# Kernel tuning notes

Hardware: AMD Instinct MI355X
Metric: run time of the kernel (lower is better)

The kernel has to match this reference:

```python
import jax, jax.numpy as jnp
import numpy as np

EPS = 1e-12  # torch F.normalize eps

def _normalize(x):
    # L2-normalize along last dim, matching F.normalize(dim=-1)
    n = jnp.linalg.norm(x, axis=-1, keepdims=True)
    return x / jnp.maximum(n, EPS)

def setup_inputs() -> dict:
    key = jax.random.key(0)
    k1, k2, k3 = jax.random.split(key, 3)
    B, K, D = 32768, 8, 256
    return {
        "drone_slots": jax.random.normal(k1, (B, K, D), dtype=jnp.float32),
        "sat_slots": jax.random.normal(k2, (B, K, D), dtype=jnp.float32),
        "labels": jax.random.randint(k3, (B,), 0, 1000, dtype=jnp.int64),
        "temperature": 0.1,
    }

def reference(drone_slots, sat_slots, labels, temperature):
    # labels are unused by the original math (targets are arange(K))
    ds = _normalize(drone_slots)  # [B,K,D]
    ss = _normalize(sat_slots)    # [B,K,D]
    logits = jnp.einsum("bkd,bjd->bkj", ds, ss) / temperature  # [B,K,K]
    # cross_entropy with targets = arange(K): positive is the diagonal
    lse = jax.nn.logsumexp(logits, axis=-1)                      # [B,K]
    pos = jnp.diagonal(logits, axis1=-2, axis2=-1)               # [B,K]
    ce_per_sample = jnp.mean(lse - pos, axis=-1)                 # [B], per-sample mean-reduced CE
    return jnp.mean(ce_per_sample)                               # average over batch
```

## Files before the change

### kernel.cpp

```cpp
#include <hip/hip_runtime.h>


typedef __attribute__((ext_vector_type(8))) short bf16x8;
typedef __attribute__((ext_vector_type(4))) float f32x4;

__device__ inline short f2bf(float f) {
  union { float f; unsigned u; } v; v.f = f;
  unsigned u = v.u;
  u += 0x7fffu + ((u >> 16) & 1u);
  return (short)(u >> 16);
}

extern "C" __global__ __launch_bounds__(256)
void slot_ce_mfma(const float* __restrict__ ds, const float* __restrict__ ss,
                  const float* __restrict__ tptr, float* __restrict__ ws,
                  int ntiles) {
  const int lane = threadIdx.x & 63;
  const int wid  = (blockIdx.x * (blockDim.x >> 6)) + (threadIdx.x >> 6);
  const int m = lane & 15;
  const int h = lane >> 4;
  const float inv_t = 1.0f / tptr[0];

  float loss = 0.0f;

  if (wid < ntiles) {
    const float4* pa = (const float4*)(ds + (size_t)wid * 4096);
    const float4* pb = (const float4*)(ss + (size_t)wid * 4096);
    const int base = m * 64 + h * 2;

    f32x4 acc = {0.f, 0.f, 0.f, 0.f};
    float ssqA = 0.f, ssqS = 0.f;

#pragma unroll
    for (int kb = 0; kb < 8; ++kb) {
      const int idx = base + kb * 8;
      float4 a0 = pa[idx], a1 = pa[idx + 1];
      float4 s0 = pb[idx], s1 = pb[idx + 1];

      ssqA += a0.x*a0.x + a0.y*a0.y + a0.z*a0.z + a0.w*a0.w
            + a1.x*a1.x + a1.y*a1.y + a1.z*a1.z + a1.w*a1.w;
      ssqS += s0.x*s0.x + s0.y*s0.y + s0.z*s0.z + s0.w*s0.w
            + s1.x*s1.x + s1.y*s1.y + s1.z*s1.z + s1.w*s1.w;

      bf16x8 af = { f2bf(a0.x), f2bf(a0.y), f2bf(a0.z), f2bf(a0.w),
                    f2bf(a1.x), f2bf(a1.y), f2bf(a1.z), f2bf(a1.w) };
      bf16x8 sf = { f2bf(s0.x), f2bf(s0.y), f2bf(s0.z), f2bf(s0.w),
                    f2bf(s1.x), f2bf(s1.y), f2bf(s1.z), f2bf(s1.w) };
      acc = __builtin_amdgcn_mfma_f32_16x16x32_bf16(af, sf, acc, 0, 0, 0);
    }

    ssqA += __shfl_xor(ssqA, 16, 64);
    ssqA += __shfl_xor(ssqA, 32, 64);
    ssqS += __shfl_xor(ssqS, 16, 64);
    ssqS += __shfl_xor(ssqS, 32, 64);
    float na0 = __shfl(ssqA, h * 4 + 0, 64);
    float na1 = __shfl(ssqA, h * 4 + 1, 64);
    float na2 = __shfl(ssqA, h * 4 + 2, 64);
    float na3 = __shfl(ssqA, h * 4 + 3, 64);

    float lg0 = acc[0] * rsqrtf(na0 * ssqS) * inv_t;
    float lg1 = acc[1] * rsqrtf(na1 * ssqS) * inv_t;
    float lg2 = acc[2] * rsqrtf(na2 * ssqS) * inv_t;
    float lg3 = acc[3] * rsqrtf(na3 * ssqS) * inv_t;

    float c = 0.0f;
#pragma unroll
    for (int r = 0; r < 4; ++r) {
      float lg = r == 0 ? lg0 : r == 1 ? lg1 : r == 2 ? lg2 : lg3;
      float mx = lg;
      mx = fmaxf(mx, __shfl_xor(mx, 1, 64));
      mx = fmaxf(mx, __shfl_xor(mx, 2, 64));
      mx = fmaxf(mx, __shfl_xor(mx, 4, 64));
      float e = __expf(lg - mx);
      e += __shfl_xor(e, 1, 64);
      e += __shfl_xor(e, 2, 64);
      e += __shfl_xor(e, 4, 64);
      float lse = mx + __logf(e);
      c += lse * 0.125f;
      if (4 * h + r == m) c -= lg;
    }
    if ((m >= 8) == (h >= 2)) loss = c;
  }

#pragma unroll
  for (int o = 32; o >= 1; o >>= 1) loss += __shfl_xor(loss, o, 64);
  __shared__ float red[4];
  if (lane == 0) red[threadIdx.x >> 6] = loss;
  __syncthreads();
  if (threadIdx.x == 0)
    ws[blockIdx.x] = (red[0] + red[1]) + (red[2] + red[3]);
}

extern "C" __global__ __launch_bounds__(256)
void slot_ce_finish(const float* __restrict__ ws, float* __restrict__ out,
                    int nparts, float scale) {
  __shared__ float red[256];
  float s = 0.0f;
  for (int i = threadIdx.x; i < nparts; i += 256) s += ws[i];
  red[threadIdx.x] = s;
  __syncthreads();
  for (int o = 128; o >= 1; o >>= 1) {
    if ((int)threadIdx.x < o) red[threadIdx.x] += red[threadIdx.x + o];
    __syncthreads();
  }
  if (threadIdx.x == 0) out[0] = red[0] * scale;
}

extern "C" void kernel_launch(void* const* d_in, const int* in_sizes, int n_in,
                              void* d_out, int out_size, void* d_ws, size_t ws_size,
                              hipStream_t stream) {
  const float* ds   = (const float*)d_in[0];
  const float* ss   = (const float*)d_in[1];
  const float* tptr = (const float*)d_in[3];
  float* out = (float*)d_out;
  float* ws  = (float*)d_ws;

  const int B      = in_sizes[0] / (8 * 256);
  const int ntiles = B / 2;
  const int blocks = (ntiles + 3) / 4;

  slot_ce_mfma<<<blocks, 256, 0, stream>>>(ds, ss, tptr, ws, ntiles);
  const float scale = 1.0f / (8.0f * (float)B);
  slot_ce_finish<<<1, 256, 0, stream>>>(ws, out, blocks, scale);
}
```

Before: 106.6 us.

## Hoist all tile loads up front and use packed bf16 conversion intrinsics

All 32 float4 loads per lane are issued before any compute, so every global load is in flight at once rather than interleaved with the MFMA loop. The manual round-to-nearest bf16 conversion is replaced by the __float22bfloat162_rn pair intrinsic, which may lower to packed conversion instructions on gfx950. The launch bounds gain a min-blocks hint of 2. Holding all 32 float4 values raises register pressure to about 128 VGPRs for loaded data, which could limit occupancy on this memory-bound kernel.

```diff
diff --git a/kernel.cpp b/kernel.cpp
--- a/kernel.cpp
+++ b/kernel.cpp
@@ -1,22 +1,27 @@
 #include <hip/hip_runtime.h>
+#include <hip/hip_bf16.h>
 
 
 typedef __attribute__((ext_vector_type(8))) short bf16x8;
 typedef __attribute__((ext_vector_type(4))) float f32x4;
 
-__device__ inline short f2bf(float f) {
-  union { float f; unsigned u; } v; v.f = f;
-  unsigned u = v.u;
-  u += 0x7fffu + ((u >> 16) & 1u);
-  return (short)(u >> 16);
+union BFPack { bf16x8 v; __hip_bfloat162 h[4]; };
+
+__device__ inline bf16x8 pack8(const float4& lo, const float4& hi) {
+  BFPack u;
+  u.h[0] = __float22bfloat162_rn(make_float2(lo.x, lo.y));
+  u.h[1] = __float22bfloat162_rn(make_float2(lo.z, lo.w));
+  u.h[2] = __float22bfloat162_rn(make_float2(hi.x, hi.y));
+  u.h[3] = __float22bfloat162_rn(make_float2(hi.z, hi.w));
+  return u.v;
 }
 
-extern "C" __global__ __launch_bounds__(256)
+extern "C" __global__ __launch_bounds__(256, 2)
 void slot_ce_mfma(const float* __restrict__ ds, const float* __restrict__ ss,
                   const float* __restrict__ tptr, float* __restrict__ ws,
                   int ntiles) {
   const int lane = threadIdx.x & 63;
-  const int wid  = (blockIdx.x * (blockDim.x >> 6)) + (threadIdx.x >> 6);
+  const int wid  = blockIdx.x * 4 + (threadIdx.x >> 6);
   const int m = lane & 15;
   const int h = lane >> 4;
   const float inv_t = 1.0f / tptr[0];
@@ -28,25 +33,29 @@
     const float4* pb = (const float4*)(ss + (size_t)wid * 4096);
     const int base = m * 64 + h * 2;
 
+    float4 A[16], S[16];
+#pragma unroll
+    for (int kb = 0; kb < 8; ++kb) {
+      A[2 * kb]     = pa[base + kb * 8];
+      A[2 * kb + 1] = pa[base + kb * 8 + 1];
+      S[2 * kb]     = pb[base + kb * 8];
+      S[2 * kb + 1] = pb[base + kb * 8 + 1];
+    }
+
     f32x4 acc = {0.f, 0.f, 0.f, 0.f};
     float ssqA = 0.f, ssqS = 0.f;
-
 #pragma unroll
     for (int kb = 0; kb < 8; ++kb) {
-      const int idx = base + kb * 8;
-      float4 a0 = pa[idx], a1 = pa[idx + 1];
-      float4 s0 = pb[idx], s1 = pb[idx + 1];
+      float4 a0 = A[2 * kb], a1 = A[2 * kb + 1];
+      float4 s0 = S[2 * kb], s1 = S[2 * kb + 1];
 
       ssqA += a0.x*a0.x + a0.y*a0.y + a0.z*a0.z + a0.w*a0.w
             + a1.x*a1.x + a1.y*a1.y + a1.z*a1.z + a1.w*a1.w;
       ssqS += s0.x*s0.x + s0.y*s0.y + s0.z*s0.z + s0.w*s0.w
             + s1.x*s1.x + s1.y*s1.y + s1.z*s1.z + s1.w*s1.w;
 
-      bf16x8 af = { f2bf(a0.x), f2bf(a0.y), f2bf(a0.z), f2bf(a0.w),
-                    f2bf(a1.x), f2bf(a1.y), f2bf(a1.z), f2bf(a1.w) };
-      bf16x8 sf = { f2bf(s0.x), f2bf(s0.y), f2bf(s0.z), f2bf(s0.w),
-                    f2bf(s1.x), f2bf(s1.y), f2bf(s1.z), f2bf(s1.w) };
-      acc = __builtin_amdgcn_mfma_f32_16x16x32_bf16(af, sf, acc, 0, 0, 0);
+      acc = __builtin_amdgcn_mfma_f32_16x16x32_bf16(
+          pack8(a0, a1), pack8(s0, s1), acc, 0, 0, 0);
     }
 
     ssqA += __shfl_xor(ssqA, 16, 64);
```

Measured after the change: 106.5 us. About the same (-0.1%).
